# Performance work log

Hardware: AMD Instinct MI355X
Metric: run time of the kernel (lower is better)

Reference implementation:

```python
import jax, jax.numpy as jnp
import numpy as np

B, S, D, H = 2, 2048, 1024, 16
DEPTH = D // H


def setup_inputs() -> dict:
    key = jax.random.key(0)
    ks = jax.random.split(key, 10)
    batch = jax.random.normal(ks[0], (B, S, D), dtype=jnp.float32)
    # variable-length valid rows, like padded batches in the original repo
    lengths = jax.random.randint(ks[1], (B,), S // 2, S + 1)
    mask = jnp.arange(S)[None, :] < lengths[:, None]  # (B, S) bool
    scale = 1.0 / np.sqrt(D)
    Wq = jax.random.normal(ks[2], (D, D), dtype=jnp.float32) * scale
    bq = jnp.zeros((D,), dtype=jnp.float32)
    Wk = jax.random.normal(ks[3], (D, D), dtype=jnp.float32) * scale
    bk = jnp.zeros((D,), dtype=jnp.float32)
    Wv = jax.random.normal(ks[4], (D, D), dtype=jnp.float32) * scale
    bv = jnp.zeros((D,), dtype=jnp.float32)
    Wo = jax.random.normal(ks[5], (D, D), dtype=jnp.float32) * scale
    bo = jnp.zeros((D,), dtype=jnp.float32)
    return {"batch": batch, "mask": mask, "Wq": Wq, "bq": bq, "Wk": Wk,
            "bk": bk, "Wv": Wv, "bv": bv, "Wo": Wo, "bo": bo}


def _split_heads(x):
    # (B, S, D) -> (B, H, S, depth)
    b, s, _ = x.shape
    return x.reshape(b, s, H, DEPTH).transpose(0, 2, 1, 3)


def reference(batch, mask, Wq, bq, Wk, bk, Wv, bv, Wo, bo):
    b, s, _ = batch.shape
    Q = _split_heads(batch @ Wq + bq)
    K = _split_heads(batch @ Wk + bk)
    V = _split_heads(batch @ Wv + bv)
    # scaled dot-product attention with key-padding mask
    logits = jnp.einsum('bhqd,bhkd->bhqk', Q, K) / jnp.sqrt(
        jnp.asarray(DEPTH, dtype=batch.dtype))
    neg = (~mask).astype(batch.dtype) * -1e9  # (B, S)
    logits = logits + neg[:, None, None, :]
    attn = jax.nn.softmax(logits, axis=-1)
    X = jnp.einsum('bhqk,bhkd->bhqd', attn, V)
    X = X.transpose(0, 2, 1, 3).reshape(b, s, D)
    return X @ Wo + bo
```

## Files before the change

### kernel.cpp

```cpp
#include <hip/hip_runtime.h>
#include <hip/hip_bf16.h>

#define DEV __device__ __forceinline__

typedef short bf16x8 __attribute__((ext_vector_type(8)));
typedef float f32x4  __attribute__((ext_vector_type(4)));
typedef float f32x16 __attribute__((ext_vector_type(16)));

#define Bc 2
#define Sc 2048
#define Dc 1024
#define Hc 16

#define OFF_XB    0u
#define OFF_WQKVT 8388608u
#define OFF_WOT   14680064u
#define OFF_Q     16777216u
#define OFF_K     25165824u
#define OFF_VT    33554432u
#define OFF_XA    41943040u
#define OFF_BIASC 50331648u
#define OFF_LENS  50343936u

DEV short f2bf(float f) {
    __hip_bfloat16 h = __float2bfloat16(f);
    union { __hip_bfloat16 h; short s; } u; u.h = h; return u.s;
}

DEV int cvtpk(float lo, float hi_) {
    int r;
    asm("v_cvt_pk_bf16_f32 %0, %1, %2" : "=v"(r) : "v"(lo), "v"(hi_));
    return r;
}

DEV float vexp2(float x) {
    float r;
    asm("v_exp_f32 %0, %1" : "=v"(r) : "v"(x));
    return r;
}

DEV void gload16(const void* g, void* l) {
    __builtin_amdgcn_global_load_lds((const __attribute__((address_space(1))) void*)g,
                                     (__attribute__((address_space(3))) void*)l, 16, 0, 0);
}

union I4BF { int i[4]; bf16x8 v; };

DEV bf16x8 vread(const char* Vc, int row, int kkbyte, int hi8, int rsw) {
    union { short4 h[2]; bf16x8 v; } u;
    u.h[0] = *(const short4*)(Vc + row * 128 + ((kkbyte + hi8) ^ rsw));
    u.h[1] = *(const short4*)(Vc + row * 128 + ((kkbyte + 16 + hi8) ^ rsw));
    return u.v;
}


__global__ void cast_bf16_kernel(const float* __restrict__ in, short* __restrict__ out, int n4) {
    int i = blockIdx.x * blockDim.x + threadIdx.x;
    if (i >= n4) return;
    float4 v = ((const float4*)in)[i];
    short4 o;
    o.x = f2bf(v.x); o.y = f2bf(v.y); o.z = f2bf(v.z); o.w = f2bf(v.w);
    ((short4*)out)[i] = o;
}

__global__ void wtrans_kernel(const float* __restrict__ Wq, const float* __restrict__ Wk,
                              const float* __restrict__ Wv, const float* __restrict__ Wo,
                              short* __restrict__ WQKVT, short* __restrict__ WOT) {
    const float* src; short* dst;
    int z = blockIdx.z;
    if (z == 0)      { src = Wq; dst = WQKVT; }
    else if (z == 1) { src = Wk; dst = WQKVT + 1024 * 1024; }
    else if (z == 2) { src = Wv; dst = WQKVT + 2 * 1024 * 1024; }
    else             { src = Wo; dst = WOT; }
    __shared__ float t[32][33];
    int tx = threadIdx.x, ty = threadIdx.y;
    int r0 = blockIdx.y * 32, c0 = blockIdx.x * 32;
#pragma unroll
    for (int i = 0; i < 4; i++)
        t[ty + i * 8][tx] = src[(size_t)(r0 + ty + i * 8) * Dc + c0 + tx];
    __syncthreads();
#pragma unroll
    for (int i = 0; i < 4; i++)
        dst[(size_t)(c0 + ty + i * 8) * Dc + r0 + tx] = f2bf(t[tx][ty + i * 8]);
}

__global__ void prep_small_kernel(const float* __restrict__ bq, const float* __restrict__ bk,
                                  const float* __restrict__ bv,
                                  const unsigned char* __restrict__ mask,
                                  float* __restrict__ biasc, int* __restrict__ lens) {
    int blk = blockIdx.x, t = threadIdx.x;
    if (blk == 0) {
        if (t < Dc) { biasc[t] = bq[t]; biasc[Dc + t] = bk[t]; biasc[2 * Dc + t] = bv[t]; }
        return;
    }
    int b = blk - 1;
    bool is_i32 = (mask[1] == 0);
    __shared__ int cnt;
    if (t == 0) cnt = 0;
    __syncthreads();
    int local = 0;
    for (int s = t; s < Sc; s += blockDim.x) {
        bool v = is_i32 ? (((const int*)mask)[b * Sc + s] != 0) : (mask[b * Sc + s] != 0);
        local += v ? 1 : 0;
    }
    atomicAdd(&cnt, local);
    __syncthreads();
    if (t == 0) lens[b] = cnt;
}

__global__ __launch_bounds__(256) void vtrans_kernel(const short* __restrict__ V,
                                                     short* __restrict__ VT) {
    __shared__ short t[64][65];
    int tid = threadIdx.x;
    int bh = blockIdx.y, s0 = blockIdx.x * 64;
    int rr = tid >> 2, c4 = (tid & 3) * 16;
    const short* vrow = V + ((size_t)bh * Sc + s0 + rr) * 64 + c4;
    *(bf16x8*)&t[rr][c4]     = *(const bf16x8*)(vrow);
    *(bf16x8*)&t[rr][c4 + 8] = *(const bf16x8*)(vrow + 8);
    __syncthreads();
    bf16x8 a, b2;
#pragma unroll
    for (int i = 0; i < 8; i++) { a[i] = t[c4 + i][rr]; b2[i] = t[c4 + 8 + i][rr]; }
    short* orow = VT + ((size_t)bh * 64 + rr) * Sc + s0 + c4;
    *(bf16x8*)(orow)     = a;
    *(bf16x8*)(orow + 8) = b2;
}

__global__ __launch_bounds__(256) void gemm_qkv_kernel(
    const short* __restrict__ A, const short* __restrict__ BT, const float* __restrict__ bias,
    short* __restrict__ Qp, short* __restrict__ Kp, short* __restrict__ Vp)
{
    __shared__ short As[128 * 32];
    __shared__ short Bs[128 * 32];
    int tid = threadIdx.x, lane = tid & 63, wave = tid >> 6;
    int l15 = lane & 15, lhi = lane >> 4;
    int bm = blockIdx.x, bn = blockIdx.y;
    int wm = wave >> 1, wn = wave & 1;

    const f32x4 fzero = {0.f, 0.f, 0.f, 0.f};
    f32x4 acc[4][4];
#pragma unroll
    for (int i = 0; i < 4; i++)
#pragma unroll
        for (int j = 0; j < 4; j++) acc[i][j] = fzero;

    const char* Ab = (const char*)A;
    const char* Bb = (const char*)BT;

    for (int k0 = 0; k0 < 1024; k0 += 32) {
#pragma unroll
        for (int i = 0; i < 2; i++) {
            int o = wave * 2048 + i * 1024 + lane * 16;
            int row = o >> 6, cb = o & 63;
            gload16(Ab + ((size_t)(bm * 128 + row) * 1024 + k0) * 2 + cb,
                    (char*)As + wave * 2048 + i * 1024);
            gload16(Bb + ((size_t)(bn * 128 + row) * 1024 + k0) * 2 + cb,
                    (char*)Bs + wave * 2048 + i * 1024);
        }
        __syncthreads();
        bf16x8 af[4], bfv[4];
#pragma unroll
        for (int i = 0; i < 4; i++) {
            af[i]  = *(const bf16x8*)(As + (wm * 64 + i * 16 + l15) * 32 + lhi * 8);
            bfv[i] = *(const bf16x8*)(Bs + (wn * 64 + i * 16 + l15) * 32 + lhi * 8);
        }
#pragma unroll
        for (int i = 0; i < 4; i++)
#pragma unroll
            for (int j = 0; j < 4; j++)
                acc[i][j] = __builtin_amdgcn_mfma_f32_16x16x32_bf16(af[i], bfv[j], acc[i][j], 0, 0, 0);
        __syncthreads();
    }

#pragma unroll
    for (int i = 0; i < 4; i++)
#pragma unroll
        for (int j = 0; j < 4; j++) {
            int c = bn * 128 + wn * 64 + j * 16 + l15;
            float bc = bias[c];
            int rb = bm * 128 + wm * 64 + i * 16 + 4 * lhi;
#pragma unroll
            for (int reg = 0; reg < 4; reg++) {
                int r = rb + reg;
                float v = acc[i][j][reg] + bc;
                int which = c >> 10, cc = c & 1023, h = cc >> 6, d = cc & 63;
                int b = r >> 11, s = r & 2047;
                int bh = b * Hc + h;
                if (which == 0) v *= 0.18033688f;
                short sv = f2bf(v);
                size_t idx = ((size_t)bh * Sc + s) * 64 + d;
                if (which == 0)      Qp[idx] = sv;
                else if (which == 1) Kp[idx] = sv;
                else                 Vp[idx] = sv;
            }
        }
}

__global__ __launch_bounds__(256) void gemm_out_kernel(
    const short* __restrict__ A, const short* __restrict__ BT, const float* __restrict__ bias,
    float* __restrict__ outF)
{
    __shared__ short As[128 * 32];
    __shared__ short Bs[64 * 32];
    int tid = threadIdx.x, lane = tid & 63, wave = tid >> 6;
    int l15 = lane & 15, lhi = lane >> 4;
    int bm = blockIdx.x, bn = blockIdx.y;

    const f32x4 fzero = {0.f, 0.f, 0.f, 0.f};
    f32x4 acc[2][4];
#pragma unroll
    for (int i = 0; i < 2; i++)
#pragma unroll
        for (int j = 0; j < 4; j++) acc[i][j] = fzero;

    const char* Ab = (const char*)A;
    const char* Bb = (const char*)BT;

    for (int k0 = 0; k0 < 1024; k0 += 32) {
#pragma unroll
        for (int i = 0; i < 2; i++) {
            int o = wave * 2048 + i * 1024 + lane * 16;
            int row = o >> 6, cb = o & 63;
            gload16(Ab + ((size_t)(bm * 128 + row) * 1024 + k0) * 2 + cb,
                    (char*)As + wave * 2048 + i * 1024);
        }
        {
            int o = wave * 1024 + lane * 16;
            int row = o >> 6, cb = o & 63;
            gload16(Bb + ((size_t)(bn * 64 + row) * 1024 + k0) * 2 + cb,
                    (char*)Bs + wave * 1024);
        }
        __syncthreads();
        bf16x8 af[2], bfv[4];
#pragma unroll
        for (int i = 0; i < 2; i++)
            af[i] = *(const bf16x8*)(As + (wave * 32 + i * 16 + l15) * 32 + lhi * 8);
#pragma unroll
        for (int j = 0; j < 4; j++)
            bfv[j] = *(const bf16x8*)(Bs + (j * 16 + l15) * 32 + lhi * 8);
#pragma unroll
        for (int i = 0; i < 2; i++)
#pragma unroll
            for (int j = 0; j < 4; j++)
                acc[i][j] = __builtin_amdgcn_mfma_f32_16x16x32_bf16(af[i], bfv[j], acc[i][j], 0, 0, 0);
        __syncthreads();
    }

#pragma unroll
    for (int i = 0; i < 2; i++)
#pragma unroll
        for (int j = 0; j < 4; j++) {
            int c = bn * 64 + j * 16 + l15;
            float bc = bias[c];
            int rb = bm * 128 + wave * 32 + i * 16 + 4 * lhi;
#pragma unroll
            for (int reg = 0; reg < 4; reg++)
                outF[(size_t)(rb + reg) * Dc + c] = acc[i][j][reg] + bc;
        }
}

__global__ __launch_bounds__(256) void attn_kernel(
    const short* __restrict__ Qp, const short* __restrict__ Kp, const short* __restrict__ VTp,
    const int* __restrict__ lens, short* __restrict__ Xout)
{
    int tid = threadIdx.x, lane = tid & 63, wave = tid >> 6;
    int l31 = lane & 31, hi = lane >> 5;

    int orig = blockIdx.x;
    int xcd = orig & 7, idx = orig >> 3;
    int j = idx & 3, bx = idx >> 2;
    int bh = ((j >> 1) << 4) + xcd * 2 + (j & 1);
    int b = bh >> 4, h = bh & 15;
    int q0 = bx * 128 + wave * 32;

    __shared__ short Kt[2][64 * 64];
    __shared__ short Vt[2][64 * 64];

    const short* Qb  = Qp + (size_t)bh * Sc * 64;
    const char*  Kb  = (const char*)(Kp + (size_t)bh * Sc * 64);
    const char*  VTb = (const char*)(VTp + (size_t)bh * 64 * Sc);

    bf16x8 qf[4];
#pragma unroll
    for (int kk = 0; kk < 4; kk++)
        qf[kk] = *(const bf16x8*)(Qb + (size_t)(q0 + l31) * 64 + kk * 16 + hi * 8);

    f32x16 xacc0, xacc1;
#pragma unroll
    for (int r = 0; r < 16; r++) { xacc0[r] = 0.f; xacc1[r] = 0.f; }
    float lreg = 0.f;

    int len = lens[b];
    int nt = (len + 63) >> 6;
    int rsw = (l31 & 7) << 4;
    int hi8 = hi * 8;

#define STAGE(bufi, kt_)                                                              \
    {                                                                                 \
        int k0_ = (kt_) * 64;                                                         \
        _Pragma("unroll")                                                             \
        for (int i = 0; i < 2; i++) {                                                 \
            int o = wave * 2048 + i * 1024 + lane * 16;                               \
            int row = o >> 7, cb = o & 127;                                           \
            int scb = cb ^ ((row & 7) << 4);                                          \
            gload16(Kb + (size_t)(k0_ + row) * 128 + scb,                             \
                    (char*)&Kt[bufi][0] + wave * 2048 + i * 1024);                    \
            gload16(VTb + (size_t)row * (Sc * 2) + (size_t)k0_ * 2 + scb,             \
                    (char*)&Vt[bufi][0] + wave * 2048 + i * 1024);                    \
        }                                                                             \
    }

#define DOHALF(Kc, Vc, ROFF, KBASE, KT)                                               \
    {                                                                                 \
        f32x16 s;                                                                     \
        _Pragma("unroll")                                                             \
        for (int r = 0; r < 16; r++) s[r] = 0.f;                                      \
        __builtin_amdgcn_s_setprio(1);                                                \
        _Pragma("unroll")                                                             \
        for (int kk = 0; kk < 4; kk++) {                                              \
            bf16x8 kf = *(const bf16x8*)((Kc) + (ROFF + l31) * 128 +                  \
                                         ((kk * 32 + hi * 16) ^ rsw));                \
            s = __builtin_amdgcn_mfma_f32_32x32x16_bf16(kf, qf[kk], s, 0, 0, 0);      \
        }                                                                             \
        __builtin_amdgcn_s_setprio(0);                                                \
        if ((KT) == nt - 1) {                                                         \
            int rem = len - (KT) * 64;                                                \
            if (rem < (KBASE) + 32) {                                                 \
                _Pragma("unroll")                                                     \
                for (int r = 0; r < 16; r++) {                                        \
                    int key0 = (KBASE) + 4 * hi + (r & 3) + 8 * (r >> 2);             \
                    if (key0 >= rem) s[r] = -3.0e38f;                                 \
                }                                                                     \
            }                                                                         \
        }                                                                             \
        _Pragma("unroll")                                                             \
        for (int r = 0; r < 16; r++) s[r] = vexp2(s[r]);                              \
        {                 \
            float a0 = s[0] + s[1],   a1 = s[2] + s[3];                               \
            float a2 = s[4] + s[5],   a3 = s[6] + s[7];                               \
            float a4 = s[8] + s[9],   a5 = s[10] + s[11];                             \
            float a6 = s[12] + s[13], a7 = s[14] + s[15];                             \
            float b0 = a0 + a1, b1 = a2 + a3, b2 = a4 + a5, b3 = a6 + a7;             \
            lreg += (b0 + b1) + (b2 + b3);                                            \
        }                                                                             \
        I4BF u, w;                                                                    \
        u.i[0] = cvtpk(s[0], s[1]);   u.i[1] = cvtpk(s[2], s[3]);                     \
        u.i[2] = cvtpk(s[4], s[5]);   u.i[3] = cvtpk(s[6], s[7]);                     \
        w.i[0] = cvtpk(s[8], s[9]);   w.i[1] = cvtpk(s[10], s[11]);                   \
        w.i[2] = cvtpk(s[12], s[13]); w.i[3] = cvtpk(s[14], s[15]);                   \
        __builtin_amdgcn_s_setprio(1);                                                \
        {                                                                             \
            bf16x8 v0 = vread((Vc), l31,      (KBASE) * 2,      hi8, rsw);            \
            bf16x8 v1 = vread((Vc), 32 + l31, (KBASE) * 2,      hi8, rsw);            \
            xacc0 = __builtin_amdgcn_mfma_f32_32x32x16_bf16(v0, u.v, xacc0, 0, 0, 0); \
            xacc1 = __builtin_amdgcn_mfma_f32_32x32x16_bf16(v1, u.v, xacc1, 0, 0, 0); \
            bf16x8 v2 = vread((Vc), l31,      (KBASE) * 2 + 32, hi8, rsw);            \
            bf16x8 v3 = vread((Vc), 32 + l31, (KBASE) * 2 + 32, hi8, rsw);            \
            xacc0 = __builtin_amdgcn_mfma_f32_32x32x16_bf16(v2, w.v, xacc0, 0, 0, 0); \
            xacc1 = __builtin_amdgcn_mfma_f32_32x32x16_bf16(v3, w.v, xacc1, 0, 0, 0); \
        }                                                                             \
        __builtin_amdgcn_s_setprio(0);                                                \
    }

#define DOTILE(BUFI, KT)                                                              \
    {                                                                                 \
        const char* Kc_ = (const char*)&Kt[BUFI][0];                                  \
        const char* Vc_ = (const char*)&Vt[BUFI][0];                                  \
        DOHALF(Kc_, Vc_, 0, 0, KT);                                                   \
        DOHALF(Kc_, Vc_, 32, 32, KT);                                                 \
    }

    STAGE(0, 0);
    __syncthreads();

    int kt = 0;
    while (kt + 2 <= nt) {
        if (kt + 1 < nt) STAGE(1, kt + 1);
        DOTILE(0, kt);
        __syncthreads();
        if (kt + 2 < nt) STAGE(0, kt + 2);
        DOTILE(1, kt + 1);
        __syncthreads();
        kt += 2;
    }
    if (kt < nt) DOTILE(0, kt);

    float lfull = lreg + __shfl_xor(lreg, 32, 64);
    float rl = 1.0f / lfull;
    short* orow = Xout + (size_t)(b * Sc + q0 + l31) * Dc + h * 64;
#pragma unroll
    for (int g = 0; g < 4; g++) {
        short4 o;
        o.x = f2bf(xacc0[4 * g + 0] * rl);
        o.y = f2bf(xacc0[4 * g + 1] * rl);
        o.z = f2bf(xacc0[4 * g + 2] * rl);
        o.w = f2bf(xacc0[4 * g + 3] * rl);
        *(short4*)(orow + 4 * hi + 8 * g) = o;
    }
#pragma unroll
    for (int g = 0; g < 4; g++) {
        short4 o;
        o.x = f2bf(xacc1[4 * g + 0] * rl);
        o.y = f2bf(xacc1[4 * g + 1] * rl);
        o.z = f2bf(xacc1[4 * g + 2] * rl);
        o.w = f2bf(xacc1[4 * g + 3] * rl);
        *(short4*)(orow + 32 + 4 * hi + 8 * g) = o;
    }
}


extern "C" void kernel_launch(void* const* d_in, const int* in_sizes, int n_in,
                              void* d_out, int out_size, void* d_ws, size_t ws_size,
                              hipStream_t stream) {
    const float* batch = (const float*)d_in[0];
    const unsigned char* mask = (const unsigned char*)d_in[1];
    const float* Wq = (const float*)d_in[2];
    const float* bq = (const float*)d_in[3];
    const float* Wk = (const float*)d_in[4];
    const float* bk = (const float*)d_in[5];
    const float* Wv = (const float*)d_in[6];
    const float* bv = (const float*)d_in[7];
    const float* Wo = (const float*)d_in[8];
    const float* bo = (const float*)d_in[9];

    char* ws = (char*)d_ws;
    short* XB    = (short*)(ws + OFF_XB);
    short* WQKVT = (short*)(ws + OFF_WQKVT);
    short* WOT   = (short*)(ws + OFF_WOT);
    short* Qb    = (short*)(ws + OFF_Q);
    short* Kb    = (short*)(ws + OFF_K);
    short* VTb   = (short*)(ws + OFF_VT);
    short* XAb   = (short*)(ws + OFF_XA);
    float* BIASC = (float*)(ws + OFF_BIASC);
    int*   LENS  = (int*)(ws + OFF_LENS);
    short* Vscr  = (short*)d_out;

    cast_bf16_kernel<<<4096, 256, 0, stream>>>(batch, XB, 1048576);
    wtrans_kernel<<<dim3(32, 32, 4), dim3(32, 8), 0, stream>>>(Wq, Wk, Wv, Wo, WQKVT, WOT);
    prep_small_kernel<<<3, 1024, 0, stream>>>(bq, bk, bv, mask, BIASC, LENS);

    gemm_qkv_kernel<<<dim3(32, 24), 256, 0, stream>>>(XB, WQKVT, BIASC, Qb, Kb, Vscr);
    vtrans_kernel<<<dim3(32, 32), 256, 0, stream>>>(Vscr, VTb);
    attn_kernel<<<512, 256, 0, stream>>>(Qb, Kb, VTb, LENS, XAb);
    gemm_out_kernel<<<dim3(32, 16), 256, 0, stream>>>(XAb, WOT, bo, (float*)d_out);
}
```

Before: 124.7 us.

## Fuse prep kernels, shrink attention blocks, and widen V LDS reads

Merges the cast, weight-transpose and bias/mask prep kernels into one launch to cut launch overhead. The attention kernel now runs 128-thread blocks with 64 queries each over twice as many blocks, and its staging loop is adjusted to match. V is permuted at transpose time so each V fragment comes from one 16-byte LDS read instead of two 8-byte reads. The first QK MFMA takes a zero vector directly instead of an explicitly zeroed accumulator. Smaller blocks reload K/V tiles for fewer queries, so global traffic per query goes up.

```diff
diff --git a/kernel.cpp b/kernel.cpp
--- a/kernel.cpp
+++ b/kernel.cpp
@@ -46,66 +46,69 @@
 
 union I4BF { int i[4]; bf16x8 v; };
 
-DEV bf16x8 vread(const char* Vc, int row, int kkbyte, int hi8, int rsw) {
-    union { short4 h[2]; bf16x8 v; } u;
-    u.h[0] = *(const short4*)(Vc + row * 128 + ((kkbyte + hi8) ^ rsw));
-    u.h[1] = *(const short4*)(Vc + row * 128 + ((kkbyte + 16 + hi8) ^ rsw));
-    return u.v;
-}
-
-
-__global__ void cast_bf16_kernel(const float* __restrict__ in, short* __restrict__ out, int n4) {
-    int i = blockIdx.x * blockDim.x + threadIdx.x;
-    if (i >= n4) return;
-    float4 v = ((const float4*)in)[i];
-    short4 o;
-    o.x = f2bf(v.x); o.y = f2bf(v.y); o.z = f2bf(v.z); o.w = f2bf(v.w);
-    ((short4*)out)[i] = o;
-}
-
-__global__ void wtrans_kernel(const float* __restrict__ Wq, const float* __restrict__ Wk,
-                              const float* __restrict__ Wv, const float* __restrict__ Wo,
-                              short* __restrict__ WQKVT, short* __restrict__ WOT) {
-    const float* src; short* dst;
-    int z = blockIdx.z;
-    if (z == 0)      { src = Wq; dst = WQKVT; }
-    else if (z == 1) { src = Wk; dst = WQKVT + 1024 * 1024; }
-    else if (z == 2) { src = Wv; dst = WQKVT + 2 * 1024 * 1024; }
-    else             { src = Wo; dst = WOT; }
-    __shared__ float t[32][33];
-    int tx = threadIdx.x, ty = threadIdx.y;
-    int r0 = blockIdx.y * 32, c0 = blockIdx.x * 32;
-#pragma unroll
-    for (int i = 0; i < 4; i++)
-        t[ty + i * 8][tx] = src[(size_t)(r0 + ty + i * 8) * Dc + c0 + tx];
-    __syncthreads();
-#pragma unroll
-    for (int i = 0; i < 4; i++)
-        dst[(size_t)(c0 + ty + i * 8) * Dc + r0 + tx] = f2bf(t[tx][ty + i * 8]);
-}
-
-__global__ void prep_small_kernel(const float* __restrict__ bq, const float* __restrict__ bk,
-                                  const float* __restrict__ bv,
-                                  const unsigned char* __restrict__ mask,
-                                  float* __restrict__ biasc, int* __restrict__ lens) {
+DEV bf16x8 vread(const char* Vc, int row, int grp, int hi16, int rsw) {
+    return *(const bf16x8*)(Vc + row * 128 + ((grp + hi16) ^ rsw));
+}
+
+__global__ __launch_bounds__(256) void prep_all_kernel(
+    const float* __restrict__ batch,
+    const float* __restrict__ Wq, const float* __restrict__ Wk,
+    const float* __restrict__ Wv, const float* __restrict__ Wo,
+    const float* __restrict__ bq, const float* __restrict__ bk, const float* __restrict__ bv,
+    const unsigned char* __restrict__ mask,
+    short* __restrict__ XB, short* __restrict__ WQKVT, short* __restrict__ WOT,
+    float* __restrict__ biasc, int* __restrict__ lens)
+{
+    __shared__ float tsm[32][33];
+    __shared__ int cnt;
     int blk = blockIdx.x, t = threadIdx.x;
-    if (blk == 0) {
-        if (t < Dc) { biasc[t] = bq[t]; biasc[Dc + t] = bk[t]; biasc[2 * Dc + t] = bv[t]; }
+
+    if (blk < 4096) {
+        int i = blk * 256 + t;
+        float4 v = ((const float4*)batch)[i];
+        short4 o;
+        o.x = f2bf(v.x); o.y = f2bf(v.y); o.z = f2bf(v.z); o.w = f2bf(v.w);
+        ((short4*)XB)[i] = o;
         return;
     }
-    int b = blk - 1;
-    bool is_i32 = (mask[1] == 0);
-    __shared__ int cnt;
-    if (t == 0) cnt = 0;
-    __syncthreads();
-    int local = 0;
-    for (int s = t; s < Sc; s += blockDim.x) {
-        bool v = is_i32 ? (((const int*)mask)[b * Sc + s] != 0) : (mask[b * Sc + s] != 0);
-        local += v ? 1 : 0;
-    }
-    atomicAdd(&cnt, local);
-    __syncthreads();
-    if (t == 0) lens[b] = cnt;
+    if (blk < 8192) {
+        int w = blk - 4096, z = w >> 10, tile = w & 1023;
+        const float* src; short* dst;
+        if (z == 0)      { src = Wq; dst = WQKVT; }
+        else if (z == 1) { src = Wk; dst = WQKVT + 1024 * 1024; }
+        else if (z == 2) { src = Wv; dst = WQKVT + 2 * 1024 * 1024; }
+        else             { src = Wo; dst = WOT; }
+        int tx = t & 31, ty = t >> 5;
+        int r0 = (tile >> 5) * 32, c0 = (tile & 31) * 32;
+#pragma unroll
+        for (int i = 0; i < 4; i++)
+            tsm[ty + i * 8][tx] = src[(size_t)(r0 + ty + i * 8) * Dc + c0 + tx];
+        __syncthreads();
+#pragma unroll
+        for (int i = 0; i < 4; i++)
+            dst[(size_t)(c0 + ty + i * 8) * Dc + r0 + tx] = f2bf(tsm[tx][ty + i * 8]);
+        return;
+    }
+    if (blk == 8192) {
+        for (int i = t; i < Dc; i += 256) {
+            biasc[i] = bq[i]; biasc[Dc + i] = bk[i]; biasc[2 * Dc + i] = bv[i];
+        }
+        return;
+    }
+    {
+        int b = blk - 8193;
+        bool is_i32 = (mask[1] == 0);
+        if (t == 0) cnt = 0;
+        __syncthreads();
+        int local = 0;
+        for (int s = t; s < Sc; s += 256) {
+            bool v = is_i32 ? (((const int*)mask)[b * Sc + s] != 0) : (mask[b * Sc + s] != 0);
+            local += v ? 1 : 0;
+        }
+        atomicAdd(&cnt, local);
+        __syncthreads();
+        if (t == 0) lens[b] = cnt;
+    }
 }
 
 __global__ __launch_bounds__(256) void vtrans_kernel(const short* __restrict__ V,
@@ -120,7 +123,12 @@
     __syncthreads();
     bf16x8 a, b2;
 #pragma unroll
-    for (int i = 0; i < 8; i++) { a[i] = t[c4 + i][rr]; b2[i] = t[c4 + 8 + i][rr]; }
+    for (int i = 0; i < 4; i++) {
+        a[i]      = t[c4 + i][rr];
+        a[4 + i]  = t[c4 + 8 + i][rr];
+        b2[i]     = t[c4 + 4 + i][rr];
+        b2[4 + i] = t[c4 + 12 + i][rr];
+    }
     short* orow = VT + ((size_t)bh * 64 + rr) * Sc + s0 + c4;
     *(bf16x8*)(orow)     = a;
     *(bf16x8*)(orow + 8) = b2;
@@ -259,7 +267,7 @@
         }
 }
 
-__global__ __launch_bounds__(256) void attn_kernel(
+__global__ __launch_bounds__(128) void attn_kernel(
     const short* __restrict__ Qp, const short* __restrict__ Kp, const short* __restrict__ VTp,
     const int* __restrict__ lens, short* __restrict__ Xout)
 {
@@ -271,7 +279,7 @@
     int j = idx & 3, bx = idx >> 2;
     int bh = ((j >> 1) << 4) + xcd * 2 + (j & 1);
     int b = bh >> 4, h = bh & 15;
-    int q0 = bx * 128 + wave * 32;
+    int q0 = bx * 64 + wave * 32;
 
     __shared__ short Kt[2][64 * 64];
     __shared__ short Vt[2][64 * 64];
@@ -285,41 +293,40 @@
     for (int kk = 0; kk < 4; kk++)
         qf[kk] = *(const bf16x8*)(Qb + (size_t)(q0 + l31) * 64 + kk * 16 + hi * 8);
 
-    f32x16 xacc0, xacc1;
-#pragma unroll
-    for (int r = 0; r < 16; r++) { xacc0[r] = 0.f; xacc1[r] = 0.f; }
+    f32x16 xacc0, xacc1, FZV;
+#pragma unroll
+    for (int r = 0; r < 16; r++) { xacc0[r] = 0.f; xacc1[r] = 0.f; FZV[r] = 0.f; }
     float lreg = 0.f;
 
     int len = lens[b];
     int nt = (len + 63) >> 6;
     int rsw = (l31 & 7) << 4;
-    int hi8 = hi * 8;
+    int hi16 = hi * 16;
 
 #define STAGE(bufi, kt_)                                                              \
     {                                                                                 \
         int k0_ = (kt_) * 64;                                                         \
         _Pragma("unroll")                                                             \
-        for (int i = 0; i < 2; i++) {                                                 \
-            int o = wave * 2048 + i * 1024 + lane * 16;                               \
+        for (int i = 0; i < 4; i++) {                                                 \
+            int o = wave * 1024 + i * 2048 + lane * 16;                               \
             int row = o >> 7, cb = o & 127;                                           \
             int scb = cb ^ ((row & 7) << 4);                                          \
             gload16(Kb + (size_t)(k0_ + row) * 128 + scb,                             \
-                    (char*)&Kt[bufi][0] + wave * 2048 + i * 1024);                    \
+                    (char*)&Kt[bufi][0] + wave * 1024 + i * 2048);                    \
             gload16(VTb + (size_t)row * (Sc * 2) + (size_t)k0_ * 2 + scb,             \
-                    (char*)&Vt[bufi][0] + wave * 2048 + i * 1024);                    \
+                    (char*)&Vt[bufi][0] + wave * 1024 + i * 2048);                    \
         }                                                                             \
     }
 
 #define DOHALF(Kc, Vc, ROFF, KBASE, KT)                                               \
     {                                                                                 \
-        f32x16 s;                                                                     \
+        __builtin_amdgcn_s_setprio(1);                                                \
+        bf16x8 kf0 = *(const bf16x8*)((Kc) + (ROFF + l31) * 128 + (hi16 ^ rsw));      \
+        f32x16 s = __builtin_amdgcn_mfma_f32_32x32x16_bf16(kf0, qf[0], FZV, 0, 0, 0); \
         _Pragma("unroll")                                                             \
-        for (int r = 0; r < 16; r++) s[r] = 0.f;                                      \
-        __builtin_amdgcn_s_setprio(1);                                                \
-        _Pragma("unroll")                                                             \
-        for (int kk = 0; kk < 4; kk++) {                                              \
+        for (int kk = 1; kk < 4; kk++) {                                              \
             bf16x8 kf = *(const bf16x8*)((Kc) + (ROFF + l31) * 128 +                  \
-                                         ((kk * 32 + hi * 16) ^ rsw));                \
+                                         ((kk * 32 + hi16) ^ rsw));                   \
             s = __builtin_amdgcn_mfma_f32_32x32x16_bf16(kf, qf[kk], s, 0, 0, 0);      \
         }                                                                             \
         __builtin_amdgcn_s_setprio(0);                                                \
@@ -350,12 +357,12 @@
         w.i[2] = cvtpk(s[12], s[13]); w.i[3] = cvtpk(s[14], s[15]);                   \
         __builtin_amdgcn_s_setprio(1);                                                \
         {                                                                             \
-            bf16x8 v0 = vread((Vc), l31,      (KBASE) * 2,      hi8, rsw);            \
-            bf16x8 v1 = vread((Vc), 32 + l31, (KBASE) * 2,      hi8, rsw);            \
+            bf16x8 v0 = vread((Vc), l31,      (KBASE) * 2,      hi16, rsw);           \
+            bf16x8 v1 = vread((Vc), 32 + l31, (KBASE) * 2,      hi16, rsw);           \
             xacc0 = __builtin_amdgcn_mfma_f32_32x32x16_bf16(v0, u.v, xacc0, 0, 0, 0); \
             xacc1 = __builtin_amdgcn_mfma_f32_32x32x16_bf16(v1, u.v, xacc1, 0, 0, 0); \
-            bf16x8 v2 = vread((Vc), l31,      (KBASE) * 2 + 32, hi8, rsw);            \
-            bf16x8 v3 = vread((Vc), 32 + l31, (KBASE) * 2 + 32, hi8, rsw);            \
+            bf16x8 v2 = vread((Vc), l31,      (KBASE) * 2 + 32, hi16, rsw);           \
+            bf16x8 v3 = vread((Vc), 32 + l31, (KBASE) * 2 + 32, hi16, rsw);           \
             xacc0 = __builtin_amdgcn_mfma_f32_32x32x16_bf16(v2, w.v, xacc0, 0, 0, 0); \
             xacc1 = __builtin_amdgcn_mfma_f32_32x32x16_bf16(v3, w.v, xacc1, 0, 0, 0); \
         }                                                                             \
@@ -435,12 +442,10 @@
     int*   LENS  = (int*)(ws + OFF_LENS);
     short* Vscr  = (short*)d_out;
 
-    cast_bf16_kernel<<<4096, 256, 0, stream>>>(batch, XB, 1048576);
-    wtrans_kernel<<<dim3(32, 32, 4), dim3(32, 8), 0, stream>>>(Wq, Wk, Wv, Wo, WQKVT, WOT);
-    prep_small_kernel<<<3, 1024, 0, stream>>>(bq, bk, bv, mask, BIASC, LENS);
-
+    prep_all_kernel<<<8195, 256, 0, stream>>>(batch, Wq, Wk, Wv, Wo, bq, bk, bv, mask,
+                                              XB, WQKVT, WOT, BIASC, LENS);
     gemm_qkv_kernel<<<dim3(32, 24), 256, 0, stream>>>(XB, WQKVT, BIASC, Qb, Kb, Vscr);
     vtrans_kernel<<<dim3(32, 32), 256, 0, stream>>>(Vscr, VTb);
-    attn_kernel<<<512, 256, 0, stream>>>(Qb, Kb, VTb, LENS, XAb);
+    attn_kernel<<<1024, 128, 0, stream>>>(Qb, Kb, VTb, LENS, XAb);
     gemm_out_kernel<<<dim3(32, 16), 256, 0, stream>>>(XAb, WOT, bo, (float*)d_out);
 }
```

Result: faster. 119.0 us (-4.5%).
